# Optimization experiments

Hardware: AMD Instinct MI355X
Metric: run time of the kernel (lower is better)

Reference implementation:

```python
import jax, jax.numpy as jnp
import numpy as np

B, LB, LC, H = 8, 512, 128, 256
H2 = 2 * H
MIN_WS, N_WIN = 5, 4


def _highway(x, Wn, bn, Wl, bl, Wg, bg):
    # AllenNLP-style highway: per layer, gate * relu(nonlinear) + (1-gate) * linear
    # Wn/Wl/Wg: [L, D, D]; bn/bl/bg: [L, D]
    for i in range(Wn.shape[0]):
        g = jax.nn.sigmoid(x @ Wg[i] + bg[i])
        x = g * jax.nn.relu(x @ Wn[i] + bn[i]) + (1.0 - g) * (x @ Wl[i] + bl[i])
    return x


def _additive_scores(q, k, Wq, bq, Wk, v):
    # 'BilinearAttention' in the repo is additive: v^T tanh(Wq q + Wk k)
    # q: [..., Lq, D], k: [..., Lk, D] -> scores [..., Lq, Lk]
    wq = q @ Wq + bq
    uh = k @ Wk
    return jnp.tanh(wq[..., :, None, :] + uh[..., None, :, :]) @ v


def setup_inputs() -> dict:
    key = jax.random.key(0)
    ks = jax.random.split(key, 32)
    s2 = 1.0 / np.sqrt(H2)
    s1 = 1.0 / np.sqrt(H)
    d = {
        'b_enc_output': jax.random.normal(ks[0], (B, LB, H), jnp.float32),
        'c_enc_output': jax.random.normal(ks[1], (B, LC, H), jnp.float32),
        'c_state': jax.random.normal(ks[2], (B, 1, H), jnp.float32),
        'b_mask': jnp.ones((B, LB), bool),
        'c_mask': jnp.ones((B, LC), bool),
    }
    # b_highway / c_highway: 2 layers, each with nonlinear/linear/gate Linear(2H,2H)
    for pfx, base in (('bh', 3), ('ch', 9)):
        d[pfx + '_Wn'] = jax.random.normal(ks[base + 0], (2, H2, H2), jnp.float32) * s2
        d[pfx + '_bn'] = jnp.zeros((2, H2), jnp.float32)
        d[pfx + '_Wl'] = jax.random.normal(ks[base + 1], (2, H2, H2), jnp.float32) * s2
        d[pfx + '_bl'] = jnp.zeros((2, H2), jnp.float32)
        d[pfx + '_Wg'] = jax.random.normal(ks[base + 2], (2, H2, H2), jnp.float32) * s2
        d[pfx + '_bg'] = jnp.zeros((2, H2), jnp.float32)
    # match_attn (2H) and area_attn (H)
    d['m_Wq'] = jax.random.normal(ks[15], (H2, H2), jnp.float32) * s2
    d['m_bq'] = jnp.zeros((H2,), jnp.float32)
    d['m_Wk'] = jax.random.normal(ks[16], (H2, H2), jnp.float32) * s2
    d['m_v'] = jax.random.normal(ks[17], (H2,), jnp.float32) * s2
    d['a_Wq'] = jax.random.normal(ks[18], (H, H), jnp.float32) * s1
    d['a_bq'] = jnp.zeros((H,), jnp.float32)
    d['a_Wk'] = jax.random.normal(ks[19], (H, H), jnp.float32) * s1
    d['a_v'] = jax.random.normal(ks[20], (H,), jnp.float32) * s1
    return d


def reference(b_enc_output, c_enc_output, c_state,
              bh_Wn, bh_bn, bh_Wl, bh_bl, bh_Wg, bh_bg,
              ch_Wn, ch_bn, ch_Wl, ch_bl, ch_Wg, ch_bg,
              m_Wq, m_bq, m_Wk, m_v,
              a_Wq, a_bq, a_Wk, a_v,
              b_mask, c_mask):
    Bsz, Lb, Hd = b_enc_output.shape
    Lc = c_enc_output.shape[1]
    # match(): highway over [enc ; c_state]
    cs_b = jnp.broadcast_to(c_state, (Bsz, Lb, Hd))
    cs_c = jnp.broadcast_to(c_state, (Bsz, Lc, Hd))
    b = _highway(jnp.concatenate([b_enc_output, cs_b], -1), bh_Wn, bh_bn, bh_Wl, bh_bl, bh_Wg, bh_bg)
    c = _highway(jnp.concatenate([c_enc_output, cs_c], -1), ch_Wn, ch_bn, ch_Wl, ch_bl, ch_Wg, ch_bg)
    m = _additive_scores(b, c, m_Wq, m_bq, m_Wk, m_v)  # [B,Lb,Lc]
    m = jnp.where(c_mask[:, None, :], m, -jnp.inf)
    b_score = jnp.where(b_mask, jnp.max(m, axis=-1), 0.0)  # [B,Lb]
    # segments(): multi-scale sliding windows (unfold) + area attention
    q = c_state[:, :, None, :]  # [B,1,1,H]
    segs, scores = [], []
    for i in range(N_WIN):
        ws = MIN_WS * (i + 1)
        n_seg = (Lb - ws) // MIN_WS + 1
        idx = jnp.arange(n_seg)[:, None] * MIN_WS + jnp.arange(ws)[None, :]  # [n_seg, ws]
        bw = b_enc_output[:, idx, :]  # [B,n_seg,ws,H]
        attn = jax.nn.softmax(_additive_scores(q, bw, a_Wq, a_bq, a_Wk, a_v), axis=-1)  # [B,n_seg,1,ws]
        segs.append(jnp.einsum('bnqw,bnwh->bnh', attn, bw))
        scores.append(b_score[:, idx].sum(-1))  # [B,n_seg]
    segments = jnp.concatenate(segs, axis=1)          # [B,N,H]
    s_score = jax.nn.softmax(jnp.concatenate(scores, axis=1), axis=-1)  # [B,N]
    out = jnp.einsum('bn,bnh->bh', s_score, segments)[:, None, :]  # [B,1,H]
    return out, s_score, b_score
```

## Files before the change

### kernel.cpp

```cpp
#include <hip/hip_runtime.h>
#include <hip/hip_bf16.h>
#include <cstdint>
#include <cstddef>


typedef unsigned short ushort8 __attribute__((ext_vector_type(8)));
typedef float f32x4 __attribute__((ext_vector_type(4)));
typedef float f32x2 __attribute__((ext_vector_type(2)));

#define SS 262144

__device__ __forceinline__ float fsigmoid(float x) { return 1.0f / (1.0f + __expf(-x)); }
__device__ __forceinline__ float ftanh(float x) {
  float e = __expf(2.0f * x);
  return 1.0f - 2.0f / (e + 1.0f);
}
__device__ __forceinline__ unsigned short f2bf(float x) {
  union { float f; unsigned u; } v; v.f = x;
  unsigned r = (v.u + 0x7FFFu + ((v.u >> 16) & 1u)) >> 16;
  return (unsigned short)r;
}
__device__ __forceinline__ f32x4 mfma_bf16(ushort8 a, ushort8 b, f32x4 c) {
  asm("v_mfma_f32_16x16x32_bf16 %0, %1, %2, %0" : "+v"(c) : "v"(a), "v"(b));
  return c;
}

struct WArg { const float* s[15]; };
__global__ __launch_bounds__(256) void prep_k(WArg wa, unsigned short* __restrict__ WT,
    const float* __restrict__ benc, const float* __restrict__ cenc,
    const float* __restrict__ cs,
    unsigned short* __restrict__ XB0, unsigned short* __restrict__ XC0,
    const float* __restrict__ aWq, const float* __restrict__ abq,
    float* __restrict__ wqa) {
  __shared__ float tile[64][65];
  const int blk = blockIdx.x, t = threadIdx.x;
  if (blk < 960) {
    const int mat = blk >> 6, q = blk & 63;
    const int Kd = (mat == 14) ? 256 : 512;
    const int k0 = (q >> 3) << 6, n0 = (q & 7) << 6;
    if (mat == 14 && (k0 >= 256 || n0 >= 256)) return;
    const float* __restrict__ S = wa.s[mat];
    unsigned short* __restrict__ D = WT + (size_t)mat * SS;
#pragma unroll
    for (int i = 0; i < 16; ++i) {
      int id = i * 256 + t, r = id >> 6, c = id & 63;
      tile[r][c] = S[(size_t)(k0 + r) * Kd + (n0 + c)];
    }
    __syncthreads();
#pragma unroll
    for (int i = 0; i < 16; ++i) {
      int id = i * 256 + t, r = id >> 6, c = id & 63;
      D[(size_t)(n0 + r) * Kd + (k0 + c)] = f2bf(tile[c][r]);
    }
  } else if (blk < 3520) {
    const bool isB = blk < 3008;
    const float* enc = isB ? benc : cenc;
    unsigned short* out = isB ? XB0 : XC0;
    const int Lshift = isB ? 9 : 7;
    int i4 = (blk - (isB ? 960 : 3008)) * 256 + t;
    int row = i4 >> 7, c4 = (i4 & 127) << 2;
    float4 v;
    if (c4 < 256) v = *(const float4*)(enc + ((size_t)row << 8) + c4);
    else          v = *(const float4*)(cs + ((size_t)(row >> Lshift) << 8) + (c4 - 256));
    union { unsigned short u[4]; uint2 w; } o;
    o.u[0] = f2bf(v.x); o.u[1] = f2bf(v.y); o.u[2] = f2bf(v.z); o.u[3] = f2bf(v.w);
    *(uint2*)(out + ((size_t)row << 9) + c4) = o.w;
  } else {
    int b = blk - 3520, h = t;
    float acc = abq[h];
    for (int k = 0; k < 256; ++k) acc += cs[b * 256 + k] * aWq[k * 256 + h];
    wqa[b * 256 + h] = acc;
  }
}

struct GJob {
  const unsigned short* A; const unsigned short* W0;
  const unsigned short* W1; const unsigned short* W2;
  const float* B0; const float* B1; const float* B2;
  void* Y; int lda, N, K, nbxs , epi, nb, blk0;
};

template <int NB>
__device__ __forceinline__ void gemm_body(const GJob& j, int bx, int by,
                                          unsigned short* sm, int t) {
  const int m0 = by * 64, n0 = bx * 64;
  const int lane = t & 63, wid = t >> 6;
  const int wr = wid >> 1, wc = wid & 1;
  const int N = j.N, K = j.K, lda = j.lda;

  const int srow = t >> 3;
  const int cg = (t & 7) ^ (srow & 7);
  const unsigned short* Ag0 = j.A + (size_t)(m0 + srow) * lda + cg * 8;
  const unsigned short* Ag1 = j.A + (size_t)(m0 + 32 + srow) * lda + cg * 8;
  const unsigned short* Wp[3] = {j.W0, j.W1, j.W2};
  const unsigned short* Bg0[NB], * Bg1[NB];
#pragma unroll
  for (int p = 0; p < NB; ++p) {
    Bg0[p] = Wp[p] + (size_t)(n0 + srow) * K + cg * 8;
    Bg1[p] = Wp[p] + (size_t)(n0 + 32 + srow) * K + cg * 8;
  }
  const int d0 = t * 8, d1 = (256 + t) * 8;

  const int fl = lane & 15, lg = lane >> 4;
  int offA[2][2], offB[2][2];
#pragma unroll
  for (int f = 0; f < 2; ++f) {
    int ra = wr * 32 + f * 16 + fl;
    int rb2 = wc * 32 + f * 16 + fl;
#pragma unroll
    for (int ks = 0; ks < 2; ++ks) {
      offA[f][ks] = ra * 64 + ((((ks << 2) + lg) ^ (ra & 7)) << 3);
      offB[f][ks] = rb2 * 64 + ((((ks << 2) + lg) ^ (rb2 & 7)) << 3);
    }
  }

  f32x4 acc[NB][2][2];
#pragma unroll
  for (int p = 0; p < NB; ++p)
#pragma unroll
    for (int i = 0; i < 2; ++i)
#pragma unroll
      for (int q = 0; q < 2; ++q) acc[p][i][q] = (f32x4){0.f, 0.f, 0.f, 0.f};

  ushort8 ra0 = *(const ushort8*)Ag0, ra1 = *(const ushort8*)Ag1;
  ushort8 rb0[NB], rb1[NB];
#pragma unroll
  for (int p = 0; p < NB; ++p) { rb0[p] = *(const ushort8*)Bg0[p]; rb1[p] = *(const ushort8*)Bg1[p]; }

  for (int k0 = 0; k0 < K; k0 += 64) {
    __syncthreads();
    *(ushort8*)&sm[d0] = ra0;
    *(ushort8*)&sm[d1] = ra1;
#pragma unroll
    for (int p = 0; p < NB; ++p) {
      unsigned short* Bs = sm + (1 + p) * 4096;
      *(ushort8*)&Bs[d0] = rb0[p];
      *(ushort8*)&Bs[d1] = rb1[p];
    }
    __syncthreads();
    if (k0 + 64 < K) {
      ra0 = *(const ushort8*)(Ag0 + k0 + 64);
      ra1 = *(const ushort8*)(Ag1 + k0 + 64);
#pragma unroll
      for (int p = 0; p < NB; ++p) {
        rb0[p] = *(const ushort8*)(Bg0[p] + k0 + 64);
        rb1[p] = *(const ushort8*)(Bg1[p] + k0 + 64);
      }
    }
#pragma unroll
    for (int ks = 0; ks < 2; ++ks) {
      ushort8 a0 = *(const ushort8*)&sm[offA[0][ks]];
      ushort8 a1 = *(const ushort8*)&sm[offA[1][ks]];
#pragma unroll
      for (int p = 0; p < NB; ++p) {
        const unsigned short* Bs = sm + (1 + p) * 4096;
        ushort8 b0 = *(const ushort8*)&Bs[offB[0][ks]];
        ushort8 b1 = *(const ushort8*)&Bs[offB[1][ks]];
        acc[p][0][0] = mfma_bf16(a0, b0, acc[p][0][0]);
        acc[p][0][1] = mfma_bf16(a0, b1, acc[p][0][1]);
        acc[p][1][0] = mfma_bf16(a1, b0, acc[p][1][0]);
        acc[p][1][1] = mfma_bf16(a1, b1, acc[p][1][1]);
      }
    }
  }
  asm volatile("s_nop 7\n\ts_nop 7" ::);

#pragma unroll
  for (int mf = 0; mf < 2; ++mf) {
#pragma unroll
    for (int nf = 0; nf < 2; ++nf) {
      const int col = n0 + wc * 32 + nf * 16 + fl;
      const int row0 = m0 + wr * 32 + mf * 16 + lg * 4;
      if constexpr (NB == 3) {
        float bn = j.B0[col], bl = j.B1[col], bg = j.B2[col];
        unsigned short* Y = (unsigned short*)j.Y;
#pragma unroll
        for (int e = 0; e < 4; ++e) {
          float nv = acc[0][mf][nf][e] + bn;
          float lv = acc[1][mf][nf][e] + bl;
          float gv = fsigmoid(acc[2][mf][nf][e] + bg);
          Y[(size_t)(row0 + e) * N + col] = f2bf(gv * fmaxf(nv, 0.f) + (1.f - gv) * lv);
        }
      } else {
        float* Y = (float*)j.Y;
        if (j.epi == 2) {
          float bb = j.B0[col];
#pragma unroll
          for (int e = 0; e < 4; ++e)
            Y[(size_t)(row0 + e) * N + col] = __expf(2.0f * (acc[0][mf][nf][e] + bb));
        } else if (j.epi == 3) {
          f32x4 w;
#pragma unroll
          for (int e = 0; e < 4; ++e) w[e] = __expf(2.0f * acc[0][mf][nf][e]);
          *(f32x4*)(Y + (((size_t)(row0 >> 7)) << 16) + ((size_t)col << 7) + (row0 & 127)) = w;
        } else {
          float bb = j.B0 ? j.B0[col] : 0.f;
#pragma unroll
          for (int e = 0; e < 4; ++e)
            Y[(size_t)(row0 + e) * N + col] = acc[0][mf][nf][e] + bb;
        }
      }
    }
  }
}

__global__ __launch_bounds__(256) void mgemm3_k(GJob j0, GJob j1, GJob j2,
    int toff, int tmode,
    const float* __restrict__ p0,
    const float* __restrict__ p1,
    const float* __restrict__ p2,
    float* __restrict__ pout) {
  __shared__ unsigned short sm[4 * 4096];
  const int blk = blockIdx.x, t = threadIdx.x;
  if (blk >= toff) {
    const int rel = blk - toff;
    if (tmode == 1) {
      const int lane = t & 63, wid = t >> 6;
      const int pos = (rel << 2) + wid;
      const int b = pos >> 9;
      const int h0 = lane << 2;
      float4 u = *(const float4*)(p0 + (size_t)pos * 256 + h0);
      float4 w = *(const float4*)(p1 + b * 256 + h0);
      float4 v = *(const float4*)(p2 + h0);
      float s = ftanh(w.x + u.x) * v.x + ftanh(w.y + u.y) * v.y +
                ftanh(w.z + u.z) * v.z + ftanh(w.w + u.w) * v.w;
#pragma unroll
      for (int off = 32; off; off >>= 1) s += __shfl_xor(s, off);
      if (lane == 0) pout[pos] = s;
    } else {
      const int b = rel / 402, s = rel - b * 402;
      const int h = t;
      int i, n;
      if (s < 102)      { i = 0; n = s; }
      else if (s < 203) { i = 1; n = s - 102; }
      else if (s < 303) { i = 2; n = s - 203; }
      else              { i = 3; n = s - 303; }
      const int ws = 5 * (i + 1), start = n * 5;
      const float* tb = p0 + b * 512 + start;
      float mx = -3.0e38f;
      for (int w = 0; w < ws; ++w) mx = fmaxf(mx, tb[w]);
      float sum = 0.f;
      for (int w = 0; w < ws; ++w) sum += __expf(tb[w] - mx);
      float inv = 1.f / sum;
      float acc = 0.f;
      for (int w = 0; w < ws; ++w)
        acc += __expf(tb[w] - mx) * p1[((size_t)(b * 512 + start + w)) * 256 + h];
      pout[((size_t)(b * 402 + s)) * 256 + h] = acc * inv;
    }
    return;
  }
  GJob j = j0;
  if (blk >= j1.blk0) j = j1;
  if (blk >= j2.blk0) j = j2;
  const int rel = blk - j.blk0;
  const int bx = rel & ((1 << j.nbxs) - 1), by = rel >> j.nbxs;
  if (j.nb == 3) gemm_body<3>(j, bx, by, sm, t);
  else          gemm_body<1>(j, bx, by, sm, t);
}

__device__ __forceinline__ void ms_comp(const float* eb, const float* vbp, int h0,
    f32x2 u0, f32x2 u1, f32x2 u2, f32x2 u3,
    f32x2& a0, f32x2& a1, f32x2& a2, f32x2& a3) {
  f32x4 v4 = *(const f32x4*)(vbp + h0);
#pragma unroll
  for (int r = 0; r < 4; ++r) {
    f32x2& ar = (r == 0) ? a0 : (r == 1) ? a1 : (r == 2) ? a2 : a3;
    f32x4 e4 = *(const f32x4*)(eb + r * 512 + h0);
    ar.x = __builtin_fmaf(v4[0], __builtin_amdgcn_rcpf(__builtin_fmaf(e4[0], u0.x, 1.f)), ar.x);
    ar.y = __builtin_fmaf(v4[0], __builtin_amdgcn_rcpf(__builtin_fmaf(e4[0], u0.y, 1.f)), ar.y);
    ar.x = __builtin_fmaf(v4[1], __builtin_amdgcn_rcpf(__builtin_fmaf(e4[1], u1.x, 1.f)), ar.x);
    ar.y = __builtin_fmaf(v4[1], __builtin_amdgcn_rcpf(__builtin_fmaf(e4[1], u1.y, 1.f)), ar.y);
    ar.x = __builtin_fmaf(v4[2], __builtin_amdgcn_rcpf(__builtin_fmaf(e4[2], u2.x, 1.f)), ar.x);
    ar.y = __builtin_fmaf(v4[2], __builtin_amdgcn_rcpf(__builtin_fmaf(e4[2], u2.y, 1.f)), ar.y);
    ar.x = __builtin_fmaf(v4[3], __builtin_amdgcn_rcpf(__builtin_fmaf(e4[3], u3.x, 1.f)), ar.x);
    ar.y = __builtin_fmaf(v4[3], __builtin_amdgcn_rcpf(__builtin_fmaf(e4[3], u3.y, 1.f)), ar.y);
  }
}

__global__ __launch_bounds__(256) void mscore_k(const float* __restrict__ EW,
                                                const float* __restrict__ UHT,
                                                const float* __restrict__ mv,
                                                float* __restrict__ bscore) {
  __shared__ __align__(16) float smem[4 * 512 + 512];
  float* ews = smem;
  float* vvs = smem + 2048;
  const int t = threadIdx.x, lane = t & 63, w = t >> 6;
  const int vb = blockIdx.x;
  const int row0 = vb << 2;
  const int b = row0 >> 9;
#pragma unroll
  for (int q = 0; q < 2; ++q) {
    int f4 = q * 256 + t, r = f4 >> 7, c4 = (f4 & 127) << 2;
    *(float4*)&ews[r * 512 + c4] =
        *(const float4*)(EW + (((size_t)(row0 + r)) << 9) + c4);
  }
  if (t < 128) *(float4*)&vvs[t << 2] = *(const float4*)(mv + (t << 2));
  __syncthreads();

  const float* up = UHT + ((size_t)b << 16) + (w << 14) + (lane << 1);
  const float* eb = ews + (w << 7);
  const float* vbp = vvs + (w << 7);

  f32x2 a0 = {0.f, 0.f}, a1 = {0.f, 0.f}, a2 = {0.f, 0.f}, a3 = {0.f, 0.f};
  f32x2 uA0, uA1, uA2, uA3, uB0, uB1, uB2, uB3;
  uA0 = *(const f32x2*)(up + 0 * 128);
  uA1 = *(const f32x2*)(up + 1 * 128);
  uA2 = *(const f32x2*)(up + 2 * 128);
  uA3 = *(const f32x2*)(up + 3 * 128);
#pragma unroll
  for (int i = 0; i < 32; i += 2) {
    const int hB = (i + 1) * 4, hN = (i + 2) * 4;
    uB0 = *(const f32x2*)(up + (size_t)(hB + 0) * 128);
    uB1 = *(const f32x2*)(up + (size_t)(hB + 1) * 128);
    uB2 = *(const f32x2*)(up + (size_t)(hB + 2) * 128);
    uB3 = *(const f32x2*)(up + (size_t)(hB + 3) * 128);
    ms_comp(eb, vbp, i * 4, uA0, uA1, uA2, uA3, a0, a1, a2, a3);
    if (i + 2 < 32) {
      uA0 = *(const f32x2*)(up + (size_t)(hN + 0) * 128);
      uA1 = *(const f32x2*)(up + (size_t)(hN + 1) * 128);
      uA2 = *(const f32x2*)(up + (size_t)(hN + 2) * 128);
      uA3 = *(const f32x2*)(up + (size_t)(hN + 3) * 128);
    }
    ms_comp(eb, vbp, hB, uB0, uB1, uB2, uB3, a0, a1, a2, a3);
  }

  __syncthreads();
  float* part = smem;
  *(f32x2*)&part[((w * 4 + 0) * 128) + (lane << 1)] = a0;
  *(f32x2*)&part[((w * 4 + 1) * 128) + (lane << 1)] = a1;
  *(f32x2*)&part[((w * 4 + 2) * 128) + (lane << 1)] = a2;
  *(f32x2*)&part[((w * 4 + 3) * 128) + (lane << 1)] = a3;
  __syncthreads();

  {
    const int r = w;
    f32x2 s0 = *(const f32x2*)&part[((0 * 4 + r) * 128) + (lane << 1)];
    f32x2 s1 = *(const f32x2*)&part[((1 * 4 + r) * 128) + (lane << 1)];
    f32x2 s2 = *(const f32x2*)&part[((2 * 4 + r) * 128) + (lane << 1)];
    f32x2 s3 = *(const f32x2*)&part[((3 * 4 + r) * 128) + (lane << 1)];
    float sx = s0.x + s1.x + s2.x + s3.x;
    float sy = s0.y + s1.y + s2.y + s3.y;
    float m = fminf(sx, sy);
#pragma unroll
    for (int off = 32; off; off >>= 1) m = fminf(m, __shfl_xor(m, off));
    float V = 0.f;
#pragma unroll
    for (int k = 0; k < 8; ++k) V += vvs[lane + (k << 6)];
#pragma unroll
    for (int off = 32; off; off >>= 1) V += __shfl_xor(V, off);
    if (lane == 0) bscore[row0 + r] = V - 2.f * m;
  }
}

__global__ __launch_bounds__(256) void final_k(const float* __restrict__ bscore,
                                               const float* __restrict__ seg,
                                               float* __restrict__ dout) {
  const int b = blockIdx.x, t = threadIdx.x, lane = t & 63, wid = t >> 6;
  __shared__ float sc[402];
  __shared__ float bsc[512];
  __shared__ float redm[4], reds[4];
  for (int i = t; i < 512; i += 256) bsc[i] = bscore[b * 512 + i];
  __syncthreads();
  for (int s = t; s < 402; s += 256) {
    int i, n;
    if (s < 102)      { i = 0; n = s; }
    else if (s < 203) { i = 1; n = s - 102; }
    else if (s < 303) { i = 2; n = s - 203; }
    else              { i = 3; n = s - 303; }
    const int ws = 5 * (i + 1), start = n * 5;
    float ss = 0.f;
    for (int w = 0; w < ws; ++w) ss += bsc[start + w];
    sc[s] = ss;
  }
  __syncthreads();
  float m = -3.0e38f;
  for (int s = t; s < 402; s += 256) m = fmaxf(m, sc[s]);
#pragma unroll
  for (int off = 32; off; off >>= 1) m = fmaxf(m, __shfl_xor(m, off));
  if (lane == 0) redm[wid] = m;
  __syncthreads();
  m = fmaxf(fmaxf(redm[0], redm[1]), fmaxf(redm[2], redm[3]));
  float p = 0.f;
  for (int s = t; s < 402; s += 256) p += __expf(sc[s] - m);
#pragma unroll
  for (int off = 32; off; off >>= 1) p += __shfl_xor(p, off);
  if (lane == 0) reds[wid] = p;
  __syncthreads();
  float invS = 1.f / (reds[0] + reds[1] + reds[2] + reds[3]);
  for (int s = t; s < 402; s += 256) {
    float pv = __expf(sc[s] - m) * invS;
    dout[2048 + b * 402 + s] = pv;
    sc[s] = pv;
  }
  __syncthreads();
  float acc = 0.f;
  for (int s = 0; s < 402; ++s)
    acc += sc[s] * seg[((size_t)(b * 402 + s)) * 256 + t];
  dout[b * 256 + t] = acc;
}

extern "C" void kernel_launch(void* const* d_in, const int* in_sizes, int n_in,
                              void* d_out, int out_size, void* d_ws, size_t ws_size,
                              hipStream_t stream) {
  const float* b_enc   = (const float*)d_in[0];
  const float* c_enc   = (const float*)d_in[1];
  const float* c_state = (const float*)d_in[2];
  const float* bh_Wn = (const float*)d_in[5];
  const float* bh_bn = (const float*)d_in[6];
  const float* bh_Wl = (const float*)d_in[7];
  const float* bh_bl = (const float*)d_in[8];
  const float* bh_Wg = (const float*)d_in[9];
  const float* bh_bg = (const float*)d_in[10];
  const float* ch_Wn = (const float*)d_in[11];
  const float* ch_bn = (const float*)d_in[12];
  const float* ch_Wl = (const float*)d_in[13];
  const float* ch_bl = (const float*)d_in[14];
  const float* ch_Wg = (const float*)d_in[15];
  const float* ch_bg = (const float*)d_in[16];
  const float* m_Wq  = (const float*)d_in[17];
  const float* m_bq  = (const float*)d_in[18];
  const float* m_Wk  = (const float*)d_in[19];
  const float* m_v   = (const float*)d_in[20];
  const float* a_Wq  = (const float*)d_in[21];
  const float* a_bq  = (const float*)d_in[22];
  const float* a_Wk  = (const float*)d_in[23];
  const float* a_v   = (const float*)d_in[24];

  uint8_t* base = (uint8_t*)d_ws;
  unsigned short* WT  = (unsigned short*)(base);
  unsigned short* WTa = WT + 14 * SS;
  unsigned short* XB0 = (unsigned short*)(base + 7471104);
  unsigned short* XB1 = (unsigned short*)(base + 11665408);
  unsigned short* XC0 = (unsigned short*)(base + 15859712);
  unsigned short* XC1 = (unsigned short*)(base + 16908288);
  float* EW   = (float*)(base + 17956864);
  float* UHT  = (float*)(base + 26345472);
  float* UHA  = (float*)(base + 28442624);
  float* WQA  = (float*)(base + 32636928);
  float* T    = (float*)(base + 32645120);
  float* SEG  = (float*)(base + 32661504);

  float* out = (float*)d_out;
  float* BSC = out + 5264;

  const int LW = 262144;
  const int SENT = 1 << 30;

  WArg wa;
  wa.s[0] = bh_Wn; wa.s[1] = bh_Wn + LW;
  wa.s[2] = bh_Wl; wa.s[3] = bh_Wl + LW;
  wa.s[4] = bh_Wg; wa.s[5] = bh_Wg + LW;
  wa.s[6] = ch_Wn; wa.s[7] = ch_Wn + LW;
  wa.s[8] = ch_Wl; wa.s[9] = ch_Wl + LW;
  wa.s[10] = ch_Wg; wa.s[11] = ch_Wg + LW;
  wa.s[12] = m_Wq; wa.s[13] = m_Wk; wa.s[14] = a_Wk;

  prep_k<<<3528, 256, 0, stream>>>(wa, WT, b_enc, c_enc, c_state, XB0, XC0,
                                   a_Wq, a_bq, WQA);

  {
    GJob jb = {XB0, WT, WT + 2 * SS, WT + 4 * SS, bh_bn, bh_bl, bh_bg,
               XB1, 512, 512, 512, 3, 1, 3, 0};
    GJob jc = {XC0, WT + 6 * SS, WT + 8 * SS, WT + 10 * SS, ch_bn, ch_bl, ch_bg,
               XC1, 512, 512, 512, 3, 1, 3, 512};
    GJob ja = {XB0, WTa, nullptr, nullptr, nullptr, nullptr, nullptr,
               UHA, 512, 256, 256, 2, 0, 1, 640};
    mgemm3_k<<<896, 256, 0, stream>>>(jb, jc, ja, 896, 0,
                                      nullptr, nullptr, nullptr, nullptr);
  }
  {
    GJob jb = {XB1, WT + SS, WT + 3 * SS, WT + 5 * SS,
               bh_bn + 512, bh_bl + 512, bh_bg + 512, XB0, 512, 512, 512, 3, 1, 3, 0};
    GJob jc = {XC1, WT + 7 * SS, WT + 9 * SS, WT + 11 * SS,
               ch_bn + 512, ch_bl + 512, ch_bg + 512, XC0, 512, 512, 512, 3, 1, 3, 512};
    GJob js = jc; js.blk0 = SENT;
    mgemm3_k<<<1664, 256, 0, stream>>>(jb, jc, js, 640, 1, UHA, WQA, a_v, T);
  }
  {
    GJob je = {XB0, WT + 12 * SS, nullptr, nullptr, m_bq, nullptr, nullptr,
               EW, 512, 512, 512, 3, 2, 1, 0};
    GJob ju = {XC0, WT + 13 * SS, nullptr, nullptr, nullptr, nullptr, nullptr,
               UHT, 512, 512, 512, 3, 3, 1, 512};
    GJob js = ju; js.blk0 = SENT;
    mgemm3_k<<<3856, 256, 0, stream>>>(je, ju, js, 640, 2, T, b_enc, nullptr, SEG);
  }
  mscore_k<<<1024, 256, 0, stream>>>(EW, UHT, m_v, BSC);
  final_k<<<8, 256, 0, stream>>>(BSC, SEG, out);
}
```

Measured before the change: 140.3 us.

## Merge segment pooling, match scoring and final reduction into one tail kernel

Moves the windowed softmax pooling from the third GEMM launch into a new tail kernel that also runs the match-score blocks. The last block to finish, detected with an atomic counter, runs the final softmax and weighted sum for all batches. The intent is to remove two kernel launches and their inter-kernel gaps. In exchange it adds a memset, runs the final stage on a single block looping over 8 batches serially, and stops overlapping segment work with the GEMM tiles.

```diff
diff --git a/kernel.cpp b/kernel.cpp
--- a/kernel.cpp
+++ b/kernel.cpp
@@ -206,10 +206,8 @@
 
 __global__ __launch_bounds__(256) void mgemm3_k(GJob j0, GJob j1, GJob j2,
     int toff, int tmode,
-    const float* __restrict__ p0,
-    const float* __restrict__ p1,
-    const float* __restrict__ p2,
-    float* __restrict__ pout) {
+    const float* __restrict__ p0, const float* __restrict__ p1,
+    const float* __restrict__ p2, float* __restrict__ pout) {
   __shared__ unsigned short sm[4 * 4096];
   const int blk = blockIdx.x, t = threadIdx.x;
   if (blk >= toff) {
@@ -227,25 +225,6 @@
 #pragma unroll
       for (int off = 32; off; off >>= 1) s += __shfl_xor(s, off);
       if (lane == 0) pout[pos] = s;
-    } else {
-      const int b = rel / 402, s = rel - b * 402;
-      const int h = t;
-      int i, n;
-      if (s < 102)      { i = 0; n = s; }
-      else if (s < 203) { i = 1; n = s - 102; }
-      else if (s < 303) { i = 2; n = s - 203; }
-      else              { i = 3; n = s - 303; }
-      const int ws = 5 * (i + 1), start = n * 5;
-      const float* tb = p0 + b * 512 + start;
-      float mx = -3.0e38f;
-      for (int w = 0; w < ws; ++w) mx = fmaxf(mx, tb[w]);
-      float sum = 0.f;
-      for (int w = 0; w < ws; ++w) sum += __expf(tb[w] - mx);
-      float inv = 1.f / sum;
-      float acc = 0.f;
-      for (int w = 0; w < ws; ++w)
-        acc += __expf(tb[w] - mx) * p1[((size_t)(b * 512 + start + w)) * 256 + h];
-      pout[((size_t)(b * 402 + s)) * 256 + h] = acc * inv;
     }
     return;
   }
@@ -277,15 +256,14 @@
   }
 }
 
-__global__ __launch_bounds__(256) void mscore_k(const float* __restrict__ EW,
-                                                const float* __restrict__ UHT,
-                                                const float* __restrict__ mv,
-                                                float* __restrict__ bscore) {
-  __shared__ __align__(16) float smem[4 * 512 + 512];
+__device__ void mscore_body(int vb, int t, float* smem,
+                            const float* __restrict__ EW,
+                            const float* __restrict__ UHT,
+                            const float* __restrict__ mv,
+                            float* __restrict__ bscore) {
   float* ews = smem;
   float* vvs = smem + 2048;
-  const int t = threadIdx.x, lane = t & 63, w = t >> 6;
-  const int vb = blockIdx.x;
+  const int lane = t & 63, w = t >> 6;
   const int row0 = vb << 2;
   const int b = row0 >> 9;
 #pragma unroll
@@ -352,51 +330,101 @@
   }
 }
 
-__global__ __launch_bounds__(256) void final_k(const float* __restrict__ bscore,
-                                               const float* __restrict__ seg,
-                                               float* __restrict__ dout) {
-  const int b = blockIdx.x, t = threadIdx.x, lane = t & 63, wid = t >> 6;
-  __shared__ float sc[402];
-  __shared__ float bsc[512];
-  __shared__ float redm[4], reds[4];
-  for (int i = t; i < 512; i += 256) bsc[i] = bscore[b * 512 + i];
-  __syncthreads();
-  for (int s = t; s < 402; s += 256) {
+__device__ void final8_body(int t, float* smem,
+                            const float* __restrict__ bscore,
+                            const float* __restrict__ seg,
+                            float* __restrict__ dout) {
+  float* sc   = smem;
+  float* bsc  = smem + 402;
+  float* redm = smem + 914;
+  float* reds = smem + 918;
+  const int lane = t & 63, wid = t >> 6;
+  for (int b = 0; b < 8; ++b) {
+    __syncthreads();
+    for (int i = t; i < 512; i += 256) bsc[i] = bscore[b * 512 + i];
+    __syncthreads();
+    for (int s = t; s < 402; s += 256) {
+      int i, n;
+      if (s < 102)      { i = 0; n = s; }
+      else if (s < 203) { i = 1; n = s - 102; }
+      else if (s < 303) { i = 2; n = s - 203; }
+      else              { i = 3; n = s - 303; }
+      const int ws = 5 * (i + 1), start = n * 5;
+      float ss = 0.f;
+      for (int w = 0; w < ws; ++w) ss += bsc[start + w];
+      sc[s] = ss;
+    }
+    __syncthreads();
+    float m = -3.0e38f;
+    for (int s = t; s < 402; s += 256) m = fmaxf(m, sc[s]);
+#pragma unroll
+    for (int off = 32; off; off >>= 1) m = fmaxf(m, __shfl_xor(m, off));
+    if (lane == 0) redm[wid] = m;
+    __syncthreads();
+    m = fmaxf(fmaxf(redm[0], redm[1]), fmaxf(redm[2], redm[3]));
+    float p = 0.f;
+    for (int s = t; s < 402; s += 256) p += __expf(sc[s] - m);
+#pragma unroll
+    for (int off = 32; off; off >>= 1) p += __shfl_xor(p, off);
+    if (lane == 0) reds[wid] = p;
+    __syncthreads();
+    float invS = 1.f / (reds[0] + reds[1] + reds[2] + reds[3]);
+    for (int s = t; s < 402; s += 256) {
+      float pv = __expf(sc[s] - m) * invS;
+      dout[2048 + b * 402 + s] = pv;
+      sc[s] = pv;
+    }
+    __syncthreads();
+    float acc = 0.f;
+    for (int s = 0; s < 402; ++s)
+      acc += sc[s] * seg[((size_t)(b * 402 + s)) * 256 + t];
+    dout[b * 256 + t] = acc;
+  }
+}
+
+__global__ __launch_bounds__(256) void tail_k(
+    const float* __restrict__ T, const float* __restrict__ benc,
+    float* __restrict__ SEG,
+    const float* __restrict__ EW, const float* __restrict__ UHT,
+    const float* __restrict__ mv, float* __restrict__ bscore,
+    float* __restrict__ dout, unsigned* __restrict__ cnt) {
+  __shared__ __align__(16) float smem[2560];
+  __shared__ int lastflag;
+  const int blk = blockIdx.x, t = threadIdx.x;
+
+  if (blk < 3216) {
+    const int b = blk / 402, s = blk - b * 402;
+    const int h = t;
     int i, n;
     if (s < 102)      { i = 0; n = s; }
     else if (s < 203) { i = 1; n = s - 102; }
     else if (s < 303) { i = 2; n = s - 203; }
     else              { i = 3; n = s - 303; }
     const int ws = 5 * (i + 1), start = n * 5;
-    float ss = 0.f;
-    for (int w = 0; w < ws; ++w) ss += bsc[start + w];
-    sc[s] = ss;
-  }
+    const float* tb = T + b * 512 + start;
+    float mx = -3.0e38f;
+    for (int w = 0; w < ws; ++w) mx = fmaxf(mx, tb[w]);
+    float sum = 0.f;
+    for (int w = 0; w < ws; ++w) sum += __expf(tb[w] - mx);
+    float inv = 1.f / sum;
+    float acc = 0.f;
+    for (int w = 0; w < ws; ++w)
+      acc += __expf(tb[w] - mx) * benc[((size_t)(b * 512 + start + w)) * 256 + h];
+    SEG[((size_t)(b * 402 + s)) * 256 + h] = acc * inv;
+  } else {
+    mscore_body(blk - 3216, t, smem, EW, UHT, mv, bscore);
+  }
+
   __syncthreads();
-  float m = -3.0e38f;
-  for (int s = t; s < 402; s += 256) m = fmaxf(m, sc[s]);
-#pragma unroll
-  for (int off = 32; off; off >>= 1) m = fmaxf(m, __shfl_xor(m, off));
-  if (lane == 0) redm[wid] = m;
+  if (t == 0) {
+    __threadfence();
+    unsigned r = atomicAdd(cnt, 1u);
+    lastflag = (r == 4239u);
+    if (lastflag)
+      (void)__hip_atomic_load(cnt, __ATOMIC_ACQUIRE, __HIP_MEMORY_SCOPE_AGENT);
+  }
   __syncthreads();
-  m = fmaxf(fmaxf(redm[0], redm[1]), fmaxf(redm[2], redm[3]));
-  float p = 0.f;
-  for (int s = t; s < 402; s += 256) p += __expf(sc[s] - m);
-#pragma unroll
-  for (int off = 32; off; off >>= 1) p += __shfl_xor(p, off);
-  if (lane == 0) reds[wid] = p;
-  __syncthreads();
-  float invS = 1.f / (reds[0] + reds[1] + reds[2] + reds[3]);
-  for (int s = t; s < 402; s += 256) {
-    float pv = __expf(sc[s] - m) * invS;
-    dout[2048 + b * 402 + s] = pv;
-    sc[s] = pv;
-  }
-  __syncthreads();
-  float acc = 0.f;
-  for (int s = 0; s < 402; ++s)
-    acc += sc[s] * seg[((size_t)(b * 402 + s)) * 256 + t];
-  dout[b * 256 + t] = acc;
+  if (lastflag) final8_body(t, smem, bscore, SEG, dout);
 }
 
 extern "C" void kernel_launch(void* const* d_in, const int* in_sizes, int n_in,
@@ -439,6 +467,7 @@
   float* WQA  = (float*)(base + 32636928);
   float* T    = (float*)(base + 32645120);
   float* SEG  = (float*)(base + 32661504);
+  unsigned* CNT = (unsigned*)(base + 35954688);
 
   float* out = (float*)d_out;
   float* BSC = out + 5264;
@@ -454,6 +483,8 @@
   wa.s[8] = ch_Wl; wa.s[9] = ch_Wl + LW;
   wa.s[10] = ch_Wg; wa.s[11] = ch_Wg + LW;
   wa.s[12] = m_Wq; wa.s[13] = m_Wk; wa.s[14] = a_Wk;
+
+  hipMemsetAsync(CNT, 0, 4, stream);
 
   prep_k<<<3528, 256, 0, stream>>>(wa, WT, b_enc, c_enc, c_state, XB0, XC0,
                                    a_Wq, a_bq, WQA);
@@ -482,8 +513,8 @@
     GJob ju = {XC0, WT + 13 * SS, nullptr, nullptr, nullptr, nullptr, nullptr,
                UHT, 512, 512, 512, 3, 3, 1, 512};
     GJob js = ju; js.blk0 = SENT;
-    mgemm3_k<<<3856, 256, 0, stream>>>(je, ju, js, 640, 2, T, b_enc, nullptr, SEG);
-  }
-  mscore_k<<<1024, 256, 0, stream>>>(EW, UHT, m_v, BSC);
-  final_k<<<8, 256, 0, stream>>>(BSC, SEG, out);
-}
+    mgemm3_k<<<640, 256, 0, stream>>>(je, ju, js, 640, 0,
+                                      nullptr, nullptr, nullptr, nullptr);
+  }
+  tail_k<<<4240, 256, 0, stream>>>(T, b_enc, SEG, EW, UHT, m_v, BSC, out, CNT);
+}
```

New measurement: 396.4 us. +182.6%, slower.
